# Optimization experiments

Hardware: AMD Instinct MI355X
Metric: run time of the kernel (lower is better)

The kernel has to match this reference:

```python
import jax, jax.numpy as jnp
import numpy as np
from jax import lax

B, T, V = 128, 256, 64
HF = 32   # MLP feature-imputation hidden
CTX = 32  # context hidden
HID = 64  # LSTM hidden


def _uniform(k, shape, fan):
    s = 1.0 / np.sqrt(fan)
    return jax.random.uniform(k, shape, jnp.float32, -s, s)


def setup_inputs():
    key = jax.random.key(0)
    ks = jax.random.split(key, 40)
    values = jax.random.normal(ks[0], (B, T, V), jnp.float32)
    masks = (jax.random.uniform(ks[1], (B, T, V)) > 0.3).astype(jnp.float32)
    deltas = jax.random.uniform(ks[2], (B, T, V), jnp.float32) * 5.0
    lengths = jax.random.randint(ks[3], (B,), T // 2, T + 1)
    min_vals = jnp.min(values, axis=1, keepdims=True)
    max_vals = jnp.max(values, axis=1, keepdims=True)
    D_in = 2 * V + 2 * CTX
    return dict(
        lengths=lengths, values=values, masks=masks, deltas=deltas,
        min_vals=min_vals, max_vals=max_vals,
        W_decay=_uniform(ks[4], (V, V), V), b_decay=_uniform(ks[5], (V,), V),
        W_feat=_uniform(ks[6], (V, HF, V), V), b_feat=_uniform(ks[7], (V, HF), V),
        W_nl1=_uniform(ks[8], (HF, HF), HF), b_nl1=_uniform(ks[9], (HF,), HF),
        W_nl2=_uniform(ks[10], (1, HF), HF), b_nl2=_uniform(ks[11], (1,), HF),
        Wc1=_uniform(ks[12], (2 * CTX, 3 * V + 1), 3 * V + 1), bc1=_uniform(ks[13], (2 * CTX,), 3 * V + 1),
        Wc2=_uniform(ks[14], (CTX, 2 * CTX), 2 * CTX), bc2=_uniform(ks[15], (CTX,), 2 * CTX),
        W_ih_g=_uniform(ks[16], (3 * CTX, 2 * V), CTX), W_hh_g=_uniform(ks[17], (3 * CTX, CTX), CTX),
        b_ih_g=_uniform(ks[18], (3 * CTX,), CTX), b_hh_g=_uniform(ks[19], (3 * CTX,), CTX),
        W_init=_uniform(ks[20], (2 * HID, 2 * CTX), 2 * CTX), b_init=_uniform(ks[21], (2 * HID,), 2 * CTX),
        W_ih_f=_uniform(ks[22], (4 * HID, D_in), HID), W_hh_f=_uniform(ks[23], (4 * HID, HID), HID),
        b_ih_f=_uniform(ks[24], (4 * HID,), HID), b_hh_f=_uniform(ks[25], (4 * HID,), HID),
        W_ih_b=_uniform(ks[26], (4 * HID, D_in), HID), W_hh_b=_uniform(ks[27], (4 * HID, HID), HID),
        b_ih_b=_uniform(ks[28], (4 * HID,), HID), b_hh_b=_uniform(ks[29], (4 * HID,), HID),
        W_ri=_uniform(ks[30], (V, 2 * HID), 2 * HID), b_ri=_uniform(ks[31], (V,), 2 * HID),
        W_fu=_uniform(ks[32], (V, 2 * V), 2 * V), b_fu=_uniform(ks[33], (V,), 2 * V),
    )


def _gru(x, h, Wih, Whh, bih, bhh):
    gi = x @ Wih.T + bih
    gh = h @ Whh.T + bhh
    ir, iz, inn = jnp.split(gi, 3, axis=-1)
    hr, hz, hn = jnp.split(gh, 3, axis=-1)
    r = jax.nn.sigmoid(ir + hr)
    z = jax.nn.sigmoid(iz + hz)
    n = jnp.tanh(inn + r * hn)
    return (1.0 - z) * n + z * h


def _lstm(x, h, c, Wih, Whh, bih, bhh):
    g = x @ Wih.T + bih + h @ Whh.T + bhh
    i, f, gg, o = jnp.split(g, 4, axis=-1)
    c = jax.nn.sigmoid(f) * c + jax.nn.sigmoid(i) * jnp.tanh(gg)
    h = jax.nn.sigmoid(o) * jnp.tanh(c)
    return h, c


def _forward(lengths, values, masks, deltas, min_vals, max_vals,
             W_decay, b_decay, W_feat, b_feat, W_nl1, b_nl1, W_nl2, b_nl2,
             Wc1, bc1, Wc2, bc2, W_ih_g, W_hh_g, b_ih_g, b_hh_g,
             W_init, b_init, W_ih_f, W_hh_f, b_ih_f, b_hh_f,
             W_ih_b, W_hh_b, b_ih_b, b_hh_b, W_ri, b_ri, W_fu, b_fu):
    Bb, Tt, Vv = values.shape
    lf = lengths.astype(jnp.float32)
    pad = (jnp.arange(Tt)[None, :] + 1 <= lengths[:, None]).astype(jnp.float32)  # [B,T]

    msum = masks.sum(axis=1)                       # [B,V] observation counts
    means = values.sum(axis=1) / msum
    var = ((values - means[:, None, :]) ** 2).sum(axis=1) / (msum - 1.0)
    stdev = jnp.sqrt(var)
    missing = 1.0 - msum / lf[:, None]
    stats = jnp.concatenate([lf[:, None], means, stdev, missing], axis=1)  # [B,3V+1]

    mmn = jnp.maximum(max_vals - min_vals, 1e-8)   # [B,1,V]
    nv = (values - min_vals) / mmn
    nmeans = (means - min_vals[:, 0, :]) / mmn[:, 0, :]

    # last-observation-carried-forward x_prime
    nv_tm = jnp.swapaxes(nv, 0, 1)   # [T,B,V]
    m_tm = jnp.swapaxes(masks, 0, 1)

    def pstep(xp, xm):
        x_prev, m_prev = xm
        xp = m_prev * x_prev + (1.0 - m_prev) * xp
        return xp, xp
    _, xp_rest = lax.scan(pstep, nv_tm[0], (nv_tm[:-1], m_tm[:-1]))
    x_prime = jnp.swapaxes(jnp.concatenate([nv_tm[:1], xp_rest], axis=0), 0, 1)

    # InputTemporalDecay: F.linear(d, W*I, b) == d * diag(W) + b
    gamma = jnp.exp(-jax.nn.relu(deltas * jnp.diag(W_decay) + b_decay))
    x_decay = gamma * x_prime + (1.0 - gamma) * nmeans[:, None, :]
    x_complete = masks * nv + (1.0 - masks) * x_decay

    # context vectors
    ctx_mlp = jax.nn.relu(stats @ Wc1.T + bc1) @ Wc2.T + bc2  # [B,CTX]
    x_rnn_tm = jnp.swapaxes(jnp.concatenate([x_complete, masks], axis=-1), 0, 1)  # [T,B,2V]
    pad_tm = jnp.swapaxes(pad, 0, 1)[:, :, None]
    h0 = jnp.zeros((Bb, W_hh_g.shape[1]), values.dtype)

    def gstep(carry, inp):
        h, hn = carry
        x_t, p_t = inp
        h = _gru(x_t, h, W_ih_g, W_hh_g, b_ih_g, b_hh_g)
        hn = p_t * h + (1.0 - p_t) * hn
        return (h, hn), None
    (_, ctx_rnn), _ = lax.scan(gstep, (h0, h0), (x_rnn_tm, pad_tm))
    context = jnp.concatenate([ctx_mlp, ctx_rnn], axis=1)  # [B,2*CTX]

    hinit = context @ W_init.T + b_init  # [B,2H]
    cinit = jnp.tanh(hinit)
    Hh = hinit.shape[1] // 2
    hf0, hb0 = hinit[:, :Hh], hinit[:, Hh:]
    cf0, cb0 = cinit[:, :Hh], cinit[:, Hh:]

    ctx_bt = jnp.broadcast_to(context[:, None, :], (Bb, Tt, context.shape[1]))
    rnn_in_tm = jnp.swapaxes(jnp.concatenate([x_complete, masks, ctx_bt], axis=-1), 0, 1)  # [T,B,D]

    def fstep(carry, x):
        h, c = _lstm(x, carry[0], carry[1], W_ih_f, W_hh_f, b_ih_f, b_hh_f)
        return (h, c), h
    _, hf_rest = lax.scan(fstep, (hf0, cf0), rnn_in_tm[:-1])
    hf_all = jnp.concatenate([hf0[None], hf_rest], axis=0)  # [T,B,H]

    def bstep(carry, x):
        h, c = _lstm(x, carry[0], carry[1], W_ih_b, W_hh_b, b_ih_b, b_hh_b)
        return (h, c), h
    _, hb_rest = lax.scan(bstep, (hb0, cb0), rnn_in_tm[1:][::-1])  # t = T-1 .. 1
    hb_all = jnp.concatenate([hb0[None], hb_rest], axis=0)[::-1]   # time-aligned

    h_cat = jnp.concatenate([hf_all, hb_all], axis=-1)  # [T,B,2H]
    rnn_imp = jnp.swapaxes(h_cat @ W_ri.T + b_ri, 0, 1)  # [B,T,V]

    # per-variable masked feature imputation (no self-connection)
    eye = jnp.eye(Vv, dtype=values.dtype)
    Wm = W_feat * (1.0 - eye[:, None, :])                 # [V,HF,V]
    hidden = jnp.einsum('btv,ghv->btgh', x_complete, Wm) + b_feat  # [B,T,V,HF]
    z = jax.nn.relu(hidden) @ W_nl1.T + b_nl1
    feat_imp = (jax.nn.relu(z) @ W_nl2.T + b_nl2)[..., 0]  # [B,T,V]

    beta = jax.nn.sigmoid(jnp.concatenate([gamma, masks], axis=-1) @ W_fu.T + b_fu)
    final_imp = beta * feat_imp + (1.0 - beta) * rnn_imp

    # unnormalize all three estimates; stack as [3,B,T,V]
    out = jnp.stack([rnn_imp, feat_imp, final_imp], axis=0) * mmn[None] + min_vals[None]
    return out


def reference(lengths, values, masks, deltas, min_vals, max_vals,
              W_decay, b_decay, W_feat, b_feat, W_nl1, b_nl1, W_nl2, b_nl2,
              Wc1, bc1, Wc2, bc2, W_ih_g, W_hh_g, b_ih_g, b_hh_g,
              W_init, b_init, W_ih_f, W_hh_f, b_ih_f, b_hh_f,
              W_ih_b, W_hh_b, b_ih_b, b_hh_b, W_ri, b_ri, W_fu, b_fu):
    return _forward(lengths, values, masks, deltas, min_vals, max_vals,
                    W_decay, b_decay, W_feat, b_feat, W_nl1, b_nl1, W_nl2, b_nl2,
                    Wc1, bc1, Wc2, bc2, W_ih_g, W_hh_g, b_ih_g, b_hh_g,
                    W_init, b_init, W_ih_f, W_hh_f, b_ih_f, b_hh_f,
                    W_ih_b, W_hh_b, b_ih_b, b_hh_b, W_ri, b_ri, W_fu, b_fu)
```

## Files before the change

### kernel.cpp

```cpp
#include <hip/hip_runtime.h>
#include <hip/hip_fp16.h>

static constexpr int NB = 128;
static constexpr int NT = 256;
static constexpr int NV = 64;
static constexpr int NBT = NB * NT;
static constexpr int NBTV = NBT * NV;

typedef __attribute__((ext_vector_type(8))) short short8;
typedef __attribute__((ext_vector_type(4))) float f32x4;
typedef __attribute__((ext_vector_type(4))) float fvec4;

__device__ __forceinline__ void wave_lds_fence() {
    __builtin_amdgcn_sched_barrier(0);
    asm volatile("s_waitcnt lgkmcnt(0)" ::: "memory");
    __builtin_amdgcn_sched_barrier(0);
}

__device__ __forceinline__ void block_sync_lds() {
    __builtin_amdgcn_sched_barrier(0);
    asm volatile("s_waitcnt lgkmcnt(0)" ::: "memory");
    __builtin_amdgcn_s_barrier();
    asm volatile("" ::: "memory");
    __builtin_amdgcn_sched_barrier(0);
}

__device__ __forceinline__ unsigned short f2bf(float x) {
    unsigned int u = __float_as_uint(x);
    return (unsigned short)((u + 0x7FFFu + ((u >> 16) & 1u)) >> 16);
}
__device__ __forceinline__ float bf2f(unsigned short b) {
    return __uint_as_float(((unsigned int)b) << 16);
}
__device__ __forceinline__ unsigned short f2h(float x) {
    union { _Float16 h; unsigned short u; } c; c.h = (_Float16)x; return c.u;
}
__device__ __forceinline__ float fsigm(float x) {
    return __builtin_amdgcn_rcpf(1.0f + __expf(-x));
}
__device__ __forceinline__ float ftanh(float x) {
    return 1.0f - 2.0f * __builtin_amdgcn_rcpf(1.0f + __expf(2.0f * x));
}

__device__ __forceinline__ short8 pack8(float4 a, float4 b) {
    short8 r;
    r[0] = (short)f2bf(a.x); r[1] = (short)f2bf(a.y); r[2] = (short)f2bf(a.z); r[3] = (short)f2bf(a.w);
    r[4] = (short)f2bf(b.x); r[5] = (short)f2bf(b.y); r[6] = (short)f2bf(b.z); r[7] = (short)f2bf(b.w);
    return r;
}

__device__ __forceinline__ void dot4(float4& acc, const float4 wv, const float4 xv) {
    acc.x = fmaf(wv.x, xv.x, acc.x);
    acc.y = fmaf(wv.y, xv.y, acc.y);
    acc.z = fmaf(wv.z, xv.z, acc.z);
    acc.w = fmaf(wv.w, xv.w, acc.w);
}

__global__ __launch_bounds__(256) void k_prep(
    const float* __restrict__ Wf, const float* __restrict__ Wihf,
    const float* __restrict__ Wihb, const float* __restrict__ Wihg,
    const float* __restrict__ Whhf, const float* __restrict__ Whhb,
    const float* __restrict__ Whhg, const float* __restrict__ Wri,
    const float* __restrict__ Wfu,
    unsigned short* __restrict__ wbf, float* __restrict__ wdiag,
    unsigned short* __restrict__ wgf, unsigned short* __restrict__ wgb,
    unsigned short* __restrict__ wgg,
    unsigned short* __restrict__ whhf_h, unsigned short* __restrict__ whhb_h,
    unsigned short* __restrict__ whhg_h,
    unsigned short* __restrict__ wri_bf, unsigned short* __restrict__ wfu_bf) {
    int i = blockIdx.x * 256 + threadIdx.x;
    if (i < NV * 32 * NV) wbf[i] = f2bf(Wf[i]);
    if (i < 2048) wdiag[i] = bf2f(f2bf(Wf[i * 64 + (i >> 5)]));
    if (i < 32768) {
        int n = i >> 7, k = i & 127;
        wgf[i] = f2bf(Wihf[n * 192 + k]);
        wgb[i] = f2bf(Wihb[n * 192 + k]);
    }
    if (i < 12288) wgg[i] = f2bf(Wihg[i]);
    if (i < 16384) { whhf_h[i] = f2h(Whhf[i]); whhb_h[i] = f2h(Whhb[i]); }
    if (i < 3072) whhg_h[i] = f2h(Whhg[i]);
    if (i < 8192) { wri_bf[i] = f2bf(Wri[i]); wfu_bf[i] = f2bf(Wfu[i]); }
}

__global__ __launch_bounds__(256) void k_fill(
    const int* __restrict__ lengths,
    const float* __restrict__ values, const float* __restrict__ masks,
    const float* __restrict__ deltas, const float* __restrict__ minv,
    const float* __restrict__ maxv,
    const float* __restrict__ Wd, const float* __restrict__ bd,
    float* __restrict__ stats,
    float* __restrict__ mmn_ws, float* __restrict__ nmeans_ws,
    float* __restrict__ xcomp, unsigned short* __restrict__ gam,
    const unsigned short* __restrict__ wgg, const float* __restrict__ bihg,
    float* __restrict__ gg) {
    int b = blockIdx.x; int tid = threadIdx.x;
    int v = tid & 63; int tc = tid >> 6;
    float mn = minv[b * NV + v];
    size_t base = (size_t)b * NT * NV + v;
    __shared__ float red[3][4][64];
    __shared__ float lastv[4][64];
    __shared__ int hasf[4][64];
    __shared__ float nv0s[64];
    __shared__ float smm[64], snm[64];
    __shared__ __align__(16) unsigned short sxc[256][64];
    int t0 = tc * 64;
    float sv = 0.f, sq = 0.f, sm = 0.f;
    float last = 0.f; int has = 0;
    for (int t = t0; t < t0 + 64; t++) {
        float val = values[base + (size_t)t * NV];
        float m = masks[base + (size_t)t * NV];
        sv += val; sq += val * val; sm += m;
        if (m != 0.f) { last = val; has = 1; }
        if (tc == 0 && t == 0) nv0s[v] = val;
    }
    red[0][tc][v] = sv; red[1][tc][v] = sq; red[2][tc][v] = sm;
    lastv[tc][v] = last; hasf[tc][v] = has;
    __syncthreads();
    if (tc == 0) {
        sv = red[0][0][v] + red[0][1][v] + red[0][2][v] + red[0][3][v];
        sq = red[1][0][v] + red[1][1][v] + red[1][2][v] + red[1][3][v];
        sm = red[2][0][v] + red[2][1][v] + red[2][2][v] + red[2][3][v];
        float mean = sv / sm;
        float var = (sq - 2.0f * mean * sv + (float)NT * mean * mean) / (sm - 1.0f);
        var = fmaxf(var, 0.0f);
        float sd = sqrtf(var);
        float lf = (float)lengths[b];
        float miss = 1.0f - sm / lf;
        float mx = maxv[b * NV + v];
        float mm = fmaxf(mx - mn, 1e-8f);
        float* st = stats + b * 256;
        if (v == 0) st[0] = lf;
        st[1 + v] = mean; st[65 + v] = sd; st[129 + v] = miss;
        float nmean = (mean - mn) / mm;
        mmn_ws[b * NV + v] = mm;
        nmeans_ws[b * NV + v] = nmean;
        smm[v] = mm; snm[v] = nmean;
    }
    __syncthreads();
    float mm = smm[v];
    float nmean = snm[v];
    float wd = Wd[v * NV + v], bdv = bd[v];
    float xp = (nv0s[v] - mn) / mm;
    for (int q = tc - 1; q >= 0; q--) {
        if (hasf[q][v]) { xp = (lastv[q][v] - mn) / mm; break; }
    }
    for (int t = t0; t < t0 + 64; t++) {
        size_t i = base + (size_t)t * NV;
        float val = values[i], m = masks[i], d = deltas[i];
        float nv = (val - mn) / mm;
        float g = expf(-fmaxf(fmaf(d, wd, bdv), 0.0f));
        float xd = g * xp + (1.0f - g) * nmean;
        float xc = m * nv + (1.0f - m) * xd;
        xcomp[i] = xc; gam[i] = f2bf(g);
        sxc[t][v] = f2bf(xc);
        xp = (m != 0.f) ? nv : xp;
    }
    __syncthreads();
    int lane = tid & 63;
    int r = lane & 15, kc = lane >> 4;
    for (int tile = 0; tile < 4; tile++) {
        int trow = (tc * 4 + tile) * 16;
        int bt0 = b * NT + trow;
        short8 af0 = *(const short8*)&sxc[trow + r][kc * 8];
        short8 af1 = *(const short8*)&sxc[trow + r][32 + kc * 8];
        const float* mr = masks + ((size_t)bt0 + r) * NV + kc * 8;
        short8 af2 = pack8(*(const float4*)(mr), *(const float4*)(mr + 4));
        short8 af3 = pack8(*(const float4*)(mr + 32), *(const float4*)(mr + 36));
        #pragma unroll 3
        for (int nt = 0; nt < 6; nt++) {
            const unsigned short* w = wgg + (size_t)(nt * 16 + r) * 128 + kc * 8;
            float bias = bihg[nt * 16 + r];
            f32x4 acc = {bias, bias, bias, bias};
            acc = __builtin_amdgcn_mfma_f32_16x16x32_bf16(af0, *(const short8*)(w), acc, 0, 0, 0);
            acc = __builtin_amdgcn_mfma_f32_16x16x32_bf16(af1, *(const short8*)(w + 32), acc, 0, 0, 0);
            acc = __builtin_amdgcn_mfma_f32_16x16x32_bf16(af2, *(const short8*)(w + 64), acc, 0, 0, 0);
            acc = __builtin_amdgcn_mfma_f32_16x16x32_bf16(af3, *(const short8*)(w + 96), acc, 0, 0, 0);
            #pragma unroll
            for (int i = 0; i < 4; i++)
                gg[(size_t)(bt0 + kc * 4 + i) * 96 + nt * 16 + r] = acc[i];
        }
    }
}

#define GRU_STEP(T, GIN) { \
    const int t_ = (T); const int p_ = t_ & 1; \
    int4 raw_[4]; \
    const int4* hp_ = (const int4*)hsg[g][s]; \
    _Pragma("unroll") for (int q = 0; q < 4; q++) raw_[q] = hp_[q]; \
    const __half2* hhv_ = (const __half2*)raw_; \
    __half2 a0_ = zh2, a1_ = zh2, a2_ = zh2, a3_ = zh2; \
    _Pragma("unroll") for (int q = 0; q < 16; q += 4) { \
        a0_ = __hfma2(w2[q],     hhv_[q],     a0_); \
        a1_ = __hfma2(w2[q + 1], hhv_[q + 1], a1_); \
        a2_ = __hfma2(w2[q + 2], hhv_[q + 2], a2_); \
        a3_ = __hfma2(w2[q + 3], hhv_[q + 3], a3_); } \
    __half2 sA_ = __hadd2(__hadd2(a0_, a1_), __hadd2(a2_, a3_)); \
    float d_ = __low2float(sA_) + __high2float(sA_); \
    if (g < 2) { \
        gexg[p_][s][n][g] = GIN + bh + d_; \
    } else { \
        gexg[p_][s][n][2] = bh + d_; \
        gexg[p_][s][n][3] = GIN; \
    } \
    block_sync_lds(); \
    float qx_ = gexg[p_][s][n][0], qy_ = gexg[p_][s][n][1]; \
    float qz_ = gexg[p_][s][n][2], qw_ = gexg[p_][s][n][3]; \
    float rr_ = fsigm(qx_); \
    float zz_ = fsigm(qy_); \
    float nn_ = ftanh(qw_ + rr_ * qz_); \
    float h_ = (1.f - zz_) * nn_ + zz_ * hprev; \
    hprev = h_; \
    if (t_ < len) hn = h_; \
    hsg[g][s][n] = f2h(h_); \
    wave_lds_fence(); \
}

#define FEAT_BODY(BT0) { \
    int bt0 = (BT0); \
    int r = lane & 15, kc = lane >> 4; \
    unsigned short* hbw = hbs[wave]; \
    float* lx = ldsx[wave]; \
    float* flw = fls[wave]; \
    short8 a0, a1; \
    { \
        const float* xr = xcomp + (size_t)(bt0 + r) * NV + kc * 8; \
        a0 = pack8(*(const float4*)(xr), *(const float4*)(xr + 4)); \
        a1 = pack8(*(const float4*)(xr + 32), *(const float4*)(xr + 36)); \
    } \
    { \
        int gc0 = kc * 16; \
        const float* xr2 = xcomp + (size_t)(bt0 + r) * NV + gc0; \
        _Pragma("unroll") for (int e = 0; e < 16; e += 4) { \
            float4 p = *(const float4*)(xr2 + e); \
            lx[(gc0 + e + 0) * 16 + r] = bf2f(f2bf(p.x)); \
            lx[(gc0 + e + 1) * 16 + r] = bf2f(f2bf(p.y)); \
            lx[(gc0 + e + 2) * 16 + r] = bf2f(f2bf(p.z)); \
            lx[(gc0 + e + 3) * 16 + r] = bf2f(f2bf(p.w)); \
        } \
    } \
    short8 wb0, wb1; \
    { \
        const float* w = Wnl1 + r * 32 + kc * 8; \
        wb0 = pack8(*(const float4*)w, *(const float4*)(w + 4)); \
        const float* w2p = Wnl1 + (16 + r) * 32 + kc * 8; \
        wb1 = pack8(*(const float4*)w2p, *(const float4*)(w2p + 4)); \
    } \
    float b0i[4], b1i[4], w2a[4], w2b[4]; \
    _Pragma("unroll") for (int i = 0; i < 4; i++) { \
        b0i[i] = bnl1[kc * 4 + i]; \
        b1i[i] = bnl1[16 + kc * 4 + i]; \
        w2a[i] = Wnl2[kc * 4 + i]; \
        w2b[i] = Wnl2[16 + kc * 4 + i]; \
    } \
    float bn2 = bnl2[0]; \
    __builtin_amdgcn_wave_barrier(); \
    _Pragma("unroll 2") for (int g = 0; g < 64; g++) { \
        __builtin_amdgcn_wave_barrier(); \
        float xv[4]; \
        _Pragma("unroll") for (int i = 0; i < 4; i++) xv[i] = lx[g * 16 + kc * 4 + i]; \
        _Pragma("unroll") for (int f = 0; f < 2; f++) { \
            int n0 = g * 32 + f * 16; \
            const unsigned short* wrow = wbf + (size_t)(n0 + r) * 64; \
            short8 b0 = *(const short8*)(wrow + kc * 8); \
            short8 b1 = *(const short8*)(wrow + 32 + kc * 8); \
            f32x4 acc = {0.f, 0.f, 0.f, 0.f}; \
            acc = __builtin_amdgcn_mfma_f32_16x16x32_bf16(a0, b0, acc, 0, 0, 0); \
            acc = __builtin_amdgcn_mfma_f32_16x16x32_bf16(a1, b1, acc, 0, 0, 0); \
            int n = n0 + r; \
            float wd = wdiag[n], bs = bfeat[n]; \
            _Pragma("unroll") for (int i = 0; i < 4; i++) { \
                float h = acc[i] - xv[i] * wd + bs; \
                h = fmaxf(h, 0.0f); \
                hbw[(kc * 4 + i) * 32 + f * 16 + r] = f2bf(h); \
            } \
        } \
        __builtin_amdgcn_wave_barrier(); \
        short8 ah = *(const short8*)(hbw + r * 32 + kc * 8); \
        f32x4 zt0 = {0.f, 0.f, 0.f, 0.f}, zt1 = {0.f, 0.f, 0.f, 0.f}; \
        zt0 = __builtin_amdgcn_mfma_f32_16x16x32_bf16(wb0, ah, zt0, 0, 0, 0); \
        zt1 = __builtin_amdgcn_mfma_f32_16x16x32_bf16(wb1, ah, zt1, 0, 0, 0); \
        float p = 0.f; \
        _Pragma("unroll") for (int i = 0; i < 4; i++) { \
            p = fmaf(fmaxf(zt0[i] + b0i[i], 0.0f), w2a[i], p); \
            p = fmaf(fmaxf(zt1[i] + b1i[i], 0.0f), w2b[i], p); \
        } \
        p += __shfl_xor(p, 16, 64); \
        p += __shfl_xor(p, 32, 64); \
        if (lane < 16) flw[lane * 65 + g] = p + bn2; \
    } \
    __builtin_amdgcn_wave_barrier(); \
    _Pragma("unroll") for (int q = 0; q < 16; q++) \
        feat_out[(size_t)(bt0 + q) * NV + lane] = flw[q * 65 + lane]; \
}

__global__ __launch_bounds__(256, 1) void k_mid(
    const float* __restrict__ gg_t, const int* __restrict__ lengths,
    const unsigned short* __restrict__ whhg_h, const float* __restrict__ bhh,
    float* __restrict__ ctx,
    const float* __restrict__ stats, const float* __restrict__ Wc1,
    const float* __restrict__ bc1, const float* __restrict__ Wc2,
    const float* __restrict__ bc2,
    const float* __restrict__ xcomp, const float* __restrict__ masks,
    const unsigned short* __restrict__ wbf,
    const float* __restrict__ wdiag, const float* __restrict__ bfeat,
    const float* __restrict__ Wnl1, const float* __restrict__ bnl1,
    const float* __restrict__ Wnl2, const float* __restrict__ bnl2,
    float* __restrict__ feat_out,
    const unsigned short* __restrict__ wgf, const unsigned short* __restrict__ wgb,
    float* __restrict__ gf, float* __restrict__ gb) {
    __shared__ __align__(16) unsigned short hsg[3][2][32];
    __shared__ __align__(16) float gexg[2][2][32][5];
    __shared__ __align__(16) float ss[193];
    __shared__ float h1[64];
    __shared__ __align__(16) unsigned short hbs[4][16 * 32];
    __shared__ __align__(16) float ldsx[4][64 * 16];
    __shared__ __align__(16) float fls[4][16 * 65];

    int bx = blockIdx.x;
    int tid = threadIdx.x;

    if (bx < 64) {
        int b0 = bx * 2;
        int g = tid >> 6;
        int lane = tid & 63;
        int s = lane >> 5, n = lane & 31;
        if (g == 3) {
            for (int t = 0; t < NT; t++) block_sync_lds();
            return;
        }
        int b = b0 + s;
        const __half2 zh2 = __float2half2_rn(0.f);
        int4 w4[4];
        {
            const int4* wp = (const int4*)(whhg_h + (size_t)(g * 32 + n) * 32);
            #pragma unroll
            for (int q = 0; q < 4; q++) w4[q] = wp[q];
        }
        const __half2* w2 = (const __half2*)w4;
        float bh = bhh[g * 32 + n];
        int len = lengths[b];
        float hprev = 0.f, hn = 0.f;
        hsg[g][s][n] = f2h(0.f);
        const float* gbase = gg_t + (size_t)b * NT * 96;
        #define GGIDX(T) ((size_t)(T) * 96 + g * 32 + n)
        float gi0 = gbase[GGIDX(0)];
        float gi1 = gbase[GGIDX(1)];
        float gi2 = gbase[GGIDX(2)];
        float gi3 = gbase[GGIDX(3)];
        wave_lds_fence();
        for (int t = 0; t < 252; t += 4) {
            GRU_STEP(t, gi0)
            gi0 = gbase[GGIDX(t + 4)];
            GRU_STEP(t + 1, gi1)
            gi1 = gbase[GGIDX(t + 5)];
            GRU_STEP(t + 2, gi2)
            gi2 = gbase[GGIDX(t + 6)];
            GRU_STEP(t + 3, gi3)
            gi3 = gbase[GGIDX(t + 7)];
        }
        GRU_STEP(252, gi0)
        GRU_STEP(253, gi1)
        GRU_STEP(254, gi2)
        GRU_STEP(255, gi3)
        #undef GGIDX
        if (g == 0) ctx[(b0 + s) * 64 + 32 + n] = hn;
    } else if (bx < 192) {
        if (tid >= 64) return;
        int b = bx - 64;
        ss[tid] = stats[b * 256 + tid];
        ss[64 + tid] = stats[b * 256 + 64 + tid];
        ss[128 + tid] = stats[b * 256 + 128 + tid];
        if (tid == 0) ss[192] = stats[b * 256 + 192];
        wave_lds_fence();
        float acc = bc1[tid];
        const float* w = Wc1 + (size_t)tid * 193;
        for (int k = 0; k < 193; k++) acc = fmaf(w[k], ss[k], acc);
        h1[tid] = fmaxf(acc, 0.f);
        wave_lds_fence();
        if (tid < 32) {
            float a = bc2[tid];
            const float* w2 = Wc2 + tid * 64;
            for (int k = 0; k < 64; k++) a = fmaf(w2[k], h1[k], a);
            ctx[b * 64 + tid] = a;
        }
    } else if (bx < 448) {
        int wave = tid >> 6; int lane = tid & 63;
        FEAT_BODY((bx - 192) * 64 + wave * 16)
    } else {
        int wave = tid >> 6, lane = tid & 63;
        int bt0 = (bx - 448) * 64 + wave * 16;
        int r = lane & 15, kc = lane >> 4;
        const float* xr = xcomp + (size_t)(bt0 + r) * NV + kc * 8;
        const float* mr = masks + (size_t)(bt0 + r) * NV + kc * 8;
        short8 af0 = pack8(*(const float4*)(xr), *(const float4*)(xr + 4));
        short8 af1 = pack8(*(const float4*)(xr + 32), *(const float4*)(xr + 36));
        short8 af2 = pack8(*(const float4*)(mr), *(const float4*)(mr + 4));
        short8 af3 = pack8(*(const float4*)(mr + 32), *(const float4*)(mr + 36));
        #pragma unroll 4
        for (int nt = 0; nt < 16; nt++) {
            const unsigned short* w = wgf + (size_t)(nt * 16 + r) * 128 + kc * 8;
            f32x4 acc = {0.f, 0.f, 0.f, 0.f};
            acc = __builtin_amdgcn_mfma_f32_16x16x32_bf16(af0, *(const short8*)(w), acc, 0, 0, 0);
            acc = __builtin_amdgcn_mfma_f32_16x16x32_bf16(af1, *(const short8*)(w + 32), acc, 0, 0, 0);
            acc = __builtin_amdgcn_mfma_f32_16x16x32_bf16(af2, *(const short8*)(w + 64), acc, 0, 0, 0);
            acc = __builtin_amdgcn_mfma_f32_16x16x32_bf16(af3, *(const short8*)(w + 96), acc, 0, 0, 0);
            int col = nt * 16 + r;
            #pragma unroll
            for (int i = 0; i < 4; i++)
                gf[(size_t)(bt0 + kc * 4 + i) * 256 + col] = acc[i];
        }
        #pragma unroll 4
        for (int nt = 0; nt < 16; nt++) {
            const unsigned short* w = wgb + (size_t)(nt * 16 + r) * 128 + kc * 8;
            f32x4 acc = {0.f, 0.f, 0.f, 0.f};
            acc = __builtin_amdgcn_mfma_f32_16x16x32_bf16(af0, *(const short8*)(w), acc, 0, 0, 0);
            acc = __builtin_amdgcn_mfma_f32_16x16x32_bf16(af1, *(const short8*)(w + 32), acc, 0, 0, 0);
            acc = __builtin_amdgcn_mfma_f32_16x16x32_bf16(af2, *(const short8*)(w + 64), acc, 0, 0, 0);
            acc = __builtin_amdgcn_mfma_f32_16x16x32_bf16(af3, *(const short8*)(w + 96), acc, 0, 0, 0);
            int col = nt * 16 + r;
            #pragma unroll
            for (int i = 0; i < 4; i++)
                gb[(size_t)(bt0 + kc * 4 + i) * 256 + col] = acc[i];
        }
    }
}

#define LSTM_STEP(S, GIN) { \
    const int s_ = (S); const int p_ = s_ & 1; \
    int4 raw_[8]; \
    const int4* hp_ = (const int4*)hs[g]; \
    _Pragma("unroll") for (int q = 0; q < 8; q++) raw_[q] = hp_[q]; \
    const __half2* hhv_ = (const __half2*)raw_; \
    __half2 a0_ = zh2, a1_ = zh2, a2_ = zh2, a3_ = zh2; \
    _Pragma("unroll") for (int q = 0; q < 32; q += 4) { \
        a0_ = __hfma2(w2[q],     hhv_[q],     a0_); \
        a1_ = __hfma2(w2[q + 1], hhv_[q + 1], a1_); \
        a2_ = __hfma2(w2[q + 2], hhv_[q + 2], a2_); \
        a3_ = __hfma2(w2[q + 3], hhv_[q + 3], a3_); } \
    __half2 sA_ = __hadd2(__hadd2(a0_, a1_), __hadd2(a2_, a3_)); \
    float d_ = __low2float(sA_) + __high2float(sA_); \
    gex[p_][n][g] = GIN + ctg + d_; \
    block_sync_lds(); \
    float qx_ = gex[p_][n][0], qy_ = gex[p_][n][1]; \
    float qz_ = gex[p_][n][2], qw_ = gex[p_][n][3]; \
    float ii_ = fsigm(qx_); \
    float ff_ = fsigm(qy_); \
    float gv_ = ftanh(qz_); \
    float oo_ = fsigm(qw_); \
    c = ff_ * c + ii_ * gv_; \
    float hv_ = oo_ * ftanh(c); \
    if (g == 0) { \
        int tout_ = dir ? (NT - 2 - s_) : (s_ + 1); \
        hall[((size_t)b * NT + tout_) * NV + n] = hv_; \
    } \
    hs[g][n] = f2h(hv_); \
    wave_lds_fence(); \
}

__global__ __launch_bounds__(256, 1) void k_lstm(
    const float* __restrict__ gf, const float* __restrict__ gb,
    const float* __restrict__ ctx,
    const unsigned short* __restrict__ whhf_h, const unsigned short* __restrict__ whhb_h,
    const float* __restrict__ Wihf, const float* __restrict__ Wihb,
    const float* __restrict__ bihf, const float* __restrict__ bhhf,
    const float* __restrict__ bihb, const float* __restrict__ bhhb,
    const float* __restrict__ Wini, const float* __restrict__ bini,
    float* __restrict__ out0, float* __restrict__ out1,
    const float* __restrict__ xcomp, const unsigned short* __restrict__ wbf,
    const float* __restrict__ wdiag, const float* __restrict__ bfeat,
    const float* __restrict__ Wnl1, const float* __restrict__ bnl1,
    const float* __restrict__ Wnl2, const float* __restrict__ bnl2,
    float* __restrict__ feat_out) {
    __shared__ __align__(16) unsigned short hs[4][64];
    __shared__ __align__(16) float gex[2][64][5];
    __shared__ __align__(16) float sctx[64];
    __shared__ __align__(16) float sh0[64];
    __shared__ __align__(16) unsigned short hbs[4][16 * 32];
    __shared__ __align__(16) float ldsx[4][64 * 16];
    __shared__ __align__(16) float fls[4][16 * 65];

    int bx = blockIdx.x;
    int tid = threadIdx.x;

    if (bx >= 256) {
        int wave = tid >> 6; int lane = tid & 63;
        FEAT_BODY((bx - 256) * 64 + 16384 + wave * 16)
        return;
    }

    int dir = bx >> 7; int b = bx & 127;
    int g = tid >> 6;
    int n = tid & 63;
    const float* gates = dir ? gb : gf;
    const unsigned short* wsrc = dir ? whhb_h : whhf_h;
    float* hall = dir ? out1 : out0;
    const __half2 zh2 = __float2half2_rn(0.f);
    int4 w4[8];
    {
        const int4* wp = (const int4*)(wsrc + (size_t)(g * 64 + n) * 64);
        #pragma unroll
        for (int q = 0; q < 8; q++) w4[q] = wp[q];
    }
    const __half2* w2 = (const __half2*)w4;
    size_t gbase = (size_t)b * NT * 256 + tid;
    #define GIDX(S) (gbase + (size_t)(dir ? (NT - 1 - (S)) : (S)) * 256)
    float gi0 = gates[GIDX(0)];
    float gi1 = gates[GIDX(1)];
    float gi2 = gates[GIDX(2)];
    float gi3 = gates[GIDX(3)];
    if (tid < 64) sctx[tid] = ctx[b * 64 + tid];
    __syncthreads();
    float ctg;
    {
        const float4* wc = (const float4*)((dir ? Wihb : Wihf) + (size_t)tid * 192 + 128);
        float bias = dir ? (bihb[tid] + bhhb[tid]) : (bihf[tid] + bhhf[tid]);
        const float4* c4 = (const float4*)sctx;
        float4 a = {0, 0, 0, 0};
        #pragma unroll
        for (int q = 0; q < 16; q++) dot4(a, wc[q], c4[q]);
        ctg = bias + a.x + a.y + a.z + a.w;
    }
    if (tid < 64) {
        const float4* wi = (const float4*)(Wini + (size_t)(dir * 64 + tid) * 64);
        const float4* c4 = (const float4*)sctx;
        float4 a = {0, 0, 0, 0};
        #pragma unroll
        for (int q = 0; q < 16; q++) dot4(a, wi[q], c4[q]);
        sh0[tid] = bini[dir * 64 + tid] + a.x + a.y + a.z + a.w;
    }
    __syncthreads();
    float c;
    {
        float h0 = sh0[n];
        c = ftanh(h0);
        hs[g][n] = f2h(h0);
        if (g == 0) {
            int t0 = dir ? (NT - 1) : 0;
            hall[((size_t)b * NT + t0) * NV + n] = h0;
        }
    }
    wave_lds_fence();
    for (int sx = 0; sx < 252; sx += 4) {
        LSTM_STEP(sx, gi0)
        gi0 = gates[GIDX(sx + 4)];
        LSTM_STEP(sx + 1, gi1)
        gi1 = gates[GIDX(sx + 5)];
        LSTM_STEP(sx + 2, gi2)
        gi2 = gates[GIDX(sx + 6)];
        LSTM_STEP(sx + 3, gi3)
        gi3 = gates[GIDX(sx + 7)];
    }
    LSTM_STEP(252, gi0)
    LSTM_STEP(253, gi1)
    LSTM_STEP(254, gi2)
    #undef GIDX
}

__global__ __launch_bounds__(256) void k_post(
    const unsigned short* __restrict__ gam, const float* __restrict__ masks,
    const unsigned short* __restrict__ wri_bf, const unsigned short* __restrict__ wfu_bf,
    const float* __restrict__ bri, const float* __restrict__ bfu,
    const float* __restrict__ mmn_ws, const float* __restrict__ minv,
    float* out0, float* out1, float* out2) {
    int wave = threadIdx.x >> 6, lane = threadIdx.x & 63;
    int bt0 = blockIdx.x * 64 + wave * 16;
    int r = lane & 15, kc = lane >> 4;
    int b = bt0 >> 8;
    const float* h0r = out0 + (size_t)(bt0 + r) * NV + kc * 8;
    const float* h1r = out1 + (size_t)(bt0 + r) * NV + kc * 8;
    const unsigned short* gr = gam + (size_t)(bt0 + r) * NV + kc * 8;
    const float* mr  = masks + (size_t)(bt0 + r) * NV + kc * 8;
    short8 A0 = pack8(*(const float4*)(h0r), *(const float4*)(h0r + 4));
    short8 A1 = pack8(*(const float4*)(h0r + 32), *(const float4*)(h0r + 36));
    short8 A2 = pack8(*(const float4*)(h1r), *(const float4*)(h1r + 4));
    short8 A3 = pack8(*(const float4*)(h1r + 32), *(const float4*)(h1r + 36));
    short8 G0 = *(const short8*)(gr);
    short8 G1 = *(const short8*)(gr + 32);
    short8 M0 = pack8(*(const float4*)(mr), *(const float4*)(mr + 4));
    short8 M1 = pack8(*(const float4*)(mr + 32), *(const float4*)(mr + 36));
    #pragma unroll
    for (int nt = 0; nt < 4; nt++) {
        int n = nt * 16 + r;
        const unsigned short* wr = wri_bf + (size_t)n * 128 + kc * 8;
        const unsigned short* wf = wfu_bf + (size_t)n * 128 + kc * 8;
        float bi = bri[n], bf_ = bfu[n];
        f32x4 racc = {bi, bi, bi, bi};
        f32x4 bacc = {bf_, bf_, bf_, bf_};
        racc = __builtin_amdgcn_mfma_f32_16x16x32_bf16(A0, *(const short8*)(wr), racc, 0, 0, 0);
        racc = __builtin_amdgcn_mfma_f32_16x16x32_bf16(A1, *(const short8*)(wr + 32), racc, 0, 0, 0);
        racc = __builtin_amdgcn_mfma_f32_16x16x32_bf16(A2, *(const short8*)(wr + 64), racc, 0, 0, 0);
        racc = __builtin_amdgcn_mfma_f32_16x16x32_bf16(A3, *(const short8*)(wr + 96), racc, 0, 0, 0);
        bacc = __builtin_amdgcn_mfma_f32_16x16x32_bf16(G0, *(const short8*)(wf), bacc, 0, 0, 0);
        bacc = __builtin_amdgcn_mfma_f32_16x16x32_bf16(G1, *(const short8*)(wf + 32), bacc, 0, 0, 0);
        bacc = __builtin_amdgcn_mfma_f32_16x16x32_bf16(M0, *(const short8*)(wf + 64), bacc, 0, 0, 0);
        bacc = __builtin_amdgcn_mfma_f32_16x16x32_bf16(M1, *(const short8*)(wf + 96), bacc, 0, 0, 0);
        float mm = mmn_ws[b * NV + n], mn = minv[b * NV + n];
        #pragma unroll
        for (int i = 0; i < 4; i++) {
            int row = bt0 + kc * 4 + i;
            size_t idx = (size_t)row * NV + n;
            float rn = racc[i];
            float beta = fsigm(bacc[i]);
            float ft = out2[idx];
            float fin = beta * ft + (1.0f - beta) * rn;
            out0[idx] = fmaf(rn, mm, mn);
            out1[idx] = fmaf(ft, mm, mn);
            out2[idx] = fmaf(fin, mm, mn);
        }
    }
}

extern "C" void kernel_launch(void* const* d_in, const int* in_sizes, int n_in,
                              void* d_out, int out_size, void* d_ws, size_t ws_size,
                              hipStream_t stream) {
    const int*   lengths  = (const int*)d_in[0];
    const float* values   = (const float*)d_in[1];
    const float* masks    = (const float*)d_in[2];
    const float* deltas   = (const float*)d_in[3];
    const float* min_vals = (const float*)d_in[4];
    const float* max_vals = (const float*)d_in[5];
    const float* W_decay  = (const float*)d_in[6];
    const float* b_decay  = (const float*)d_in[7];
    const float* W_feat   = (const float*)d_in[8];
    const float* b_feat   = (const float*)d_in[9];
    const float* W_nl1    = (const float*)d_in[10];
    const float* b_nl1    = (const float*)d_in[11];
    const float* W_nl2    = (const float*)d_in[12];
    const float* b_nl2    = (const float*)d_in[13];
    const float* Wc1      = (const float*)d_in[14];
    const float* bc1      = (const float*)d_in[15];
    const float* Wc2      = (const float*)d_in[16];
    const float* bc2      = (const float*)d_in[17];
    const float* W_ih_g   = (const float*)d_in[18];
    const float* W_hh_g   = (const float*)d_in[19];
    const float* b_ih_g   = (const float*)d_in[20];
    const float* b_hh_g   = (const float*)d_in[21];
    const float* W_init   = (const float*)d_in[22];
    const float* b_init   = (const float*)d_in[23];
    const float* W_ih_f   = (const float*)d_in[24];
    const float* W_hh_f   = (const float*)d_in[25];
    const float* b_ih_f   = (const float*)d_in[26];
    const float* b_hh_f   = (const float*)d_in[27];
    const float* W_ih_b   = (const float*)d_in[28];
    const float* W_hh_b   = (const float*)d_in[29];
    const float* b_ih_b   = (const float*)d_in[30];
    const float* b_hh_b   = (const float*)d_in[31];
    const float* W_ri     = (const float*)d_in[32];
    const float* b_ri     = (const float*)d_in[33];
    const float* W_fu     = (const float*)d_in[34];
    const float* b_fu     = (const float*)d_in[35];

    float* ws = (float*)d_ws;
    float* xcomp  = ws;
    unsigned short* gam = (unsigned short*)(ws + 2097152);
    unsigned short* wri_bf = (unsigned short*)(ws + 4194304);
    unsigned short* wfu_bf = (unsigned short*)(ws + 4198400);
    float* stats  = ws + 6291456;
    float* mmn    = ws + 6324224;
    float* nmeans = ws + 6332416;
    float* ctx    = ws + 6340608;
    unsigned short* wbf = (unsigned short*)(ws + 6365184);
    float* wdiag  = ws + 6430720;
    unsigned short* wgf = (unsigned short*)(ws + 6432768);
    unsigned short* wgb = (unsigned short*)(ws + 6449152);
    unsigned short* wgg = (unsigned short*)(ws + 6465536);
    unsigned short* whhf_h = (unsigned short*)(ws + 6471680);
    unsigned short* whhb_h = (unsigned short*)(ws + 6479872);
    unsigned short* whhg_h = (unsigned short*)(ws + 6488064);
    float* gates_f = ws + 6555136;
    float* gates_b = ws + 14943744;
    float* gates_g = ws + 23332352;

    float* out0 = (float*)d_out;
    float* out1 = out0 + NBTV;
    float* out2 = out0 + 2 * NBTV;

    k_prep<<<512, 256, 0, stream>>>(W_feat, W_ih_f, W_ih_b, W_ih_g, W_hh_f, W_hh_b, W_hh_g,
                                    W_ri, W_fu,
                                    wbf, wdiag, wgf, wgb, wgg, whhf_h, whhb_h, whhg_h,
                                    wri_bf, wfu_bf);
    k_fill<<<NB, 256, 0, stream>>>(lengths, values, masks, deltas, min_vals, max_vals,
                                   W_decay, b_decay, stats, mmn, nmeans, xcomp, gam,
                                   wgg, b_ih_g, gates_g);
    k_mid<<<960, 256, 0, stream>>>(gates_g, lengths, whhg_h, b_hh_g, ctx,
                                   stats, Wc1, bc1, Wc2, bc2,
                                   xcomp, masks, wbf, wdiag, b_feat, W_nl1, b_nl1, W_nl2, b_nl2, out2,
                                   wgf, wgb, gates_f, gates_b);
    k_lstm<<<512, 256, 0, stream>>>(gates_f, gates_b, ctx, whhf_h, whhb_h,
                                    W_ih_f, W_ih_b, b_ih_f, b_hh_f, b_ih_b, b_hh_b,
                                    W_init, b_init, out0, out1,
                                    xcomp, wbf, wdiag, b_feat, W_nl1, b_nl1, W_nl2, b_nl2, out2);
    k_post<<<NBT / 64, 256, 0, stream>>>(gam, masks, wri_bf, wfu_bf, b_ri, b_fu, mmn, min_vals,
                                         out0, out1, out2);
}
```

Baseline: 251.4 us.

## Fuse forward and backward LSTM directions into one block per batch

```diff
diff --git a/kernel.cpp b/kernel.cpp
--- a/kernel.cpp
+++ b/kernel.cpp
@@ -425,35 +425,50 @@
     }
 }
 
-#define LSTM_STEP(S, GIN) { \
+#define LSTM_STEP_D(S, GI0, GI1) { \
     const int s_ = (S); const int p_ = s_ & 1; \
-    int4 raw_[8]; \
-    const int4* hp_ = (const int4*)hs[g]; \
-    _Pragma("unroll") for (int q = 0; q < 8; q++) raw_[q] = hp_[q]; \
-    const __half2* hhv_ = (const __half2*)raw_; \
+    int4 raw0_[8], raw1_[8]; \
+    const int4* hp0_ = (const int4*)hs[g][0]; \
+    const int4* hp1_ = (const int4*)hs[g][1]; \
+    _Pragma("unroll") for (int q = 0; q < 8; q++) { raw0_[q] = hp0_[q]; raw1_[q] = hp1_[q]; } \
+    const __half2* h0v_ = (const __half2*)raw0_; \
+    const __half2* h1v_ = (const __half2*)raw1_; \
     __half2 a0_ = zh2, a1_ = zh2, a2_ = zh2, a3_ = zh2; \
+    __half2 b0_ = zh2, b1_ = zh2, b2_ = zh2, b3_ = zh2; \
     _Pragma("unroll") for (int q = 0; q < 32; q += 4) { \
-        a0_ = __hfma2(w2[q],     hhv_[q],     a0_); \
-        a1_ = __hfma2(w2[q + 1], hhv_[q + 1], a1_); \
-        a2_ = __hfma2(w2[q + 2], hhv_[q + 2], a2_); \
-        a3_ = __hfma2(w2[q + 3], hhv_[q + 3], a3_); } \
+        a0_ = __hfma2(w2f[q],     h0v_[q],     a0_); \
+        a1_ = __hfma2(w2f[q + 1], h0v_[q + 1], a1_); \
+        a2_ = __hfma2(w2f[q + 2], h0v_[q + 2], a2_); \
+        a3_ = __hfma2(w2f[q + 3], h0v_[q + 3], a3_); \
+        b0_ = __hfma2(w2b[q],     h1v_[q],     b0_); \
+        b1_ = __hfma2(w2b[q + 1], h1v_[q + 1], b1_); \
+        b2_ = __hfma2(w2b[q + 2], h1v_[q + 2], b2_); \
+        b3_ = __hfma2(w2b[q + 3], h1v_[q + 3], b3_); } \
     __half2 sA_ = __hadd2(__hadd2(a0_, a1_), __hadd2(a2_, a3_)); \
-    float d_ = __low2float(sA_) + __high2float(sA_); \
-    gex[p_][n][g] = GIN + ctg + d_; \
+    __half2 sB_ = __hadd2(__hadd2(b0_, b1_), __hadd2(b2_, b3_)); \
+    float d0_ = __low2float(sA_) + __high2float(sA_); \
+    float d1_ = __low2float(sB_) + __high2float(sB_); \
+    gex[p_][0][n][g] = GI0 + ctg0 + d0_; \
+    gex[p_][1][n][g] = GI1 + ctg1 + d1_; \
     block_sync_lds(); \
-    float qx_ = gex[p_][n][0], qy_ = gex[p_][n][1]; \
-    float qz_ = gex[p_][n][2], qw_ = gex[p_][n][3]; \
-    float ii_ = fsigm(qx_); \
-    float ff_ = fsigm(qy_); \
-    float gv_ = ftanh(qz_); \
-    float oo_ = fsigm(qw_); \
-    c = ff_ * c + ii_ * gv_; \
-    float hv_ = oo_ * ftanh(c); \
+    float qx0_ = gex[p_][0][n][0], qy0_ = gex[p_][0][n][1]; \
+    float qz0_ = gex[p_][0][n][2], qw0_ = gex[p_][0][n][3]; \
+    float qx1_ = gex[p_][1][n][0], qy1_ = gex[p_][1][n][1]; \
+    float qz1_ = gex[p_][1][n][2], qw1_ = gex[p_][1][n][3]; \
+    float ii0_ = fsigm(qx0_), ii1_ = fsigm(qx1_); \
+    float ff0_ = fsigm(qy0_), ff1_ = fsigm(qy1_); \
+    float gv0_ = ftanh(qz0_), gv1_ = ftanh(qz1_); \
+    float oo0_ = fsigm(qw0_), oo1_ = fsigm(qw1_); \
+    c0 = ff0_ * c0 + ii0_ * gv0_; \
+    c1 = ff1_ * c1 + ii1_ * gv1_; \
+    float hv0_ = oo0_ * ftanh(c0); \
+    float hv1_ = oo1_ * ftanh(c1); \
     if (g == 0) { \
-        int tout_ = dir ? (NT - 2 - s_) : (s_ + 1); \
-        hall[((size_t)b * NT + tout_) * NV + n] = hv_; \
+        out0[((size_t)b * NT + (s_ + 1)) * NV + n] = hv0_; \
+        out1[((size_t)b * NT + (NT - 2 - s_)) * NV + n] = hv1_; \
     } \
-    hs[g][n] = f2h(hv_); \
+    hs[g][0][n] = f2h(hv0_); \
+    hs[g][1][n] = f2h(hv1_); \
     wave_lds_fence(); \
 }
 
@@ -471,10 +486,10 @@
     const float* __restrict__ Wnl1, const float* __restrict__ bnl1,
     const float* __restrict__ Wnl2, const float* __restrict__ bnl2,
     float* __restrict__ feat_out) {
-    __shared__ __align__(16) unsigned short hs[4][64];
-    __shared__ __align__(16) float gex[2][64][5];
+    __shared__ __align__(16) unsigned short hs[4][2][64];
+    __shared__ __align__(16) float gex[2][2][64][5];
     __shared__ __align__(16) float sctx[64];
-    __shared__ __align__(16) float sh0[64];
+    __shared__ __align__(16) float sh0[128];
     __shared__ __align__(16) unsigned short hbs[4][16 * 32];
     __shared__ __align__(16) float ldsx[4][64 * 16];
     __shared__ __align__(16) float fls[4][16 * 65];
@@ -482,78 +497,87 @@
     int bx = blockIdx.x;
     int tid = threadIdx.x;
 
-    if (bx >= 256) {
+    if (bx >= 128) {
         int wave = tid >> 6; int lane = tid & 63;
-        FEAT_BODY((bx - 256) * 64 + 16384 + wave * 16)
+        FEAT_BODY((bx - 128) * 64 + 16384 + wave * 16)
         return;
     }
 
-    int dir = bx >> 7; int b = bx & 127;
+    int b = bx;
     int g = tid >> 6;
     int n = tid & 63;
-    const float* gates = dir ? gb : gf;
-    const unsigned short* wsrc = dir ? whhb_h : whhf_h;
-    float* hall = dir ? out1 : out0;
     const __half2 zh2 = __float2half2_rn(0.f);
-    int4 w4[8];
+    int4 w4f[8], w4b[8];
     {
-        const int4* wp = (const int4*)(wsrc + (size_t)(g * 64 + n) * 64);
+        const int4* wpf = (const int4*)(whhf_h + (size_t)(g * 64 + n) * 64);
+        const int4* wpb = (const int4*)(whhb_h + (size_t)(g * 64 + n) * 64);
         #pragma unroll
-        for (int q = 0; q < 8; q++) w4[q] = wp[q];
-    }
-    const __half2* w2 = (const __half2*)w4;
-    size_t gbase = (size_t)b * NT * 256 + tid;
-    #define GIDX(S) (gbase + (size_t)(dir ? (NT - 1 - (S)) : (S)) * 256)
-    float gi0 = gates[GIDX(0)];
-    float gi1 = gates[GIDX(1)];
-    float gi2 = gates[GIDX(2)];
-    float gi3 = gates[GIDX(3)];
+        for (int q = 0; q < 8; q++) { w4f[q] = wpf[q]; w4b[q] = wpb[q]; }
+    }
+    const __half2* w2f = (const __half2*)w4f;
+    const __half2* w2b = (const __half2*)w4b;
+    size_t gbf = (size_t)b * NT * 256 + tid;
+    #define GIDX0(S) (gbf + (size_t)(S) * 256)
+    #define GIDX1(S) (gbf + (size_t)(NT - 1 - (S)) * 256)
+    float gi0_0 = gf[GIDX0(0)], gi0_1 = gb[GIDX1(0)];
+    float gi1_0 = gf[GIDX0(1)], gi1_1 = gb[GIDX1(1)];
+    float gi2_0 = gf[GIDX0(2)], gi2_1 = gb[GIDX1(2)];
+    float gi3_0 = gf[GIDX0(3)], gi3_1 = gb[GIDX1(3)];
     if (tid < 64) sctx[tid] = ctx[b * 64 + tid];
     __syncthreads();
-    float ctg;
+    float ctg0, ctg1;
     {
-        const float4* wc = (const float4*)((dir ? Wihb : Wihf) + (size_t)tid * 192 + 128);
-        float bias = dir ? (bihb[tid] + bhhb[tid]) : (bihf[tid] + bhhf[tid]);
         const float4* c4 = (const float4*)sctx;
-        float4 a = {0, 0, 0, 0};
+        const float4* wcf = (const float4*)(Wihf + (size_t)tid * 192 + 128);
+        const float4* wcb = (const float4*)(Wihb + (size_t)tid * 192 + 128);
+        float4 af = {0, 0, 0, 0}, ab = {0, 0, 0, 0};
         #pragma unroll
-        for (int q = 0; q < 16; q++) dot4(a, wc[q], c4[q]);
-        ctg = bias + a.x + a.y + a.z + a.w;
-    }
-    if (tid < 64) {
-        const float4* wi = (const float4*)(Wini + (size_t)(dir * 64 + tid) * 64);
+        for (int q = 0; q < 16; q++) {
+            float4 cv = c4[q];
+            dot4(af, wcf[q], cv);
+            dot4(ab, wcb[q], cv);
+        }
+        ctg0 = bihf[tid] + bhhf[tid] + af.x + af.y + af.z + af.w;
+        ctg1 = bihb[tid] + bhhb[tid] + ab.x + ab.y + ab.z + ab.w;
+    }
+    if (tid < 128) {
+        const float4* wi = (const float4*)(Wini + (size_t)tid * 64);
         const float4* c4 = (const float4*)sctx;
         float4 a = {0, 0, 0, 0};
         #pragma unroll
         for (int q = 0; q < 16; q++) dot4(a, wi[q], c4[q]);
-        sh0[tid] = bini[dir * 64 + tid] + a.x + a.y + a.z + a.w;
+        sh0[tid] = bini[tid] + a.x + a.y + a.z + a.w;
     }
     __syncthreads();
-    float c;
+    float c0, c1;
     {
-        float h0 = sh0[n];
-        c = ftanh(h0);
-        hs[g][n] = f2h(h0);
+        float h00 = sh0[n];
+        float h01 = sh0[64 + n];
+        c0 = ftanh(h00);
+        c1 = ftanh(h01);
+        hs[g][0][n] = f2h(h00);
+        hs[g][1][n] = f2h(h01);
         if (g == 0) {
-            int t0 = dir ? (NT - 1) : 0;
-            hall[((size_t)b * NT + t0) * NV + n] = h0;
+            out0[((size_t)b * NT + 0) * NV + n] = h00;
+            out1[((size_t)b * NT + (NT - 1)) * NV + n] = h01;
         }
     }
     wave_lds_fence();
     for (int sx = 0; sx < 252; sx += 4) {
-        LSTM_STEP(sx, gi0)
-        gi0 = gates[GIDX(sx + 4)];
-        LSTM_STEP(sx + 1, gi1)
-        gi1 = gates[GIDX(sx + 5)];
-        LSTM_STEP(sx + 2, gi2)
-        gi2 = gates[GIDX(sx + 6)];
-        LSTM_STEP(sx + 3, gi3)
-        gi3 = gates[GIDX(sx + 7)];
-    }
-    LSTM_STEP(252, gi0)
-    LSTM_STEP(253, gi1)
-    LSTM_STEP(254, gi2)
-    #undef GIDX
+        LSTM_STEP_D(sx, gi0_0, gi0_1)
+        gi0_0 = gf[GIDX0(sx + 4)]; gi0_1 = gb[GIDX1(sx + 4)];
+        LSTM_STEP_D(sx + 1, gi1_0, gi1_1)
+        gi1_0 = gf[GIDX0(sx + 5)]; gi1_1 = gb[GIDX1(sx + 5)];
+        LSTM_STEP_D(sx + 2, gi2_0, gi2_1)
+        gi2_0 = gf[GIDX0(sx + 6)]; gi2_1 = gb[GIDX1(sx + 6)];
+        LSTM_STEP_D(sx + 3, gi3_0, gi3_1)
+        gi3_0 = gf[GIDX0(sx + 7)]; gi3_1 = gb[GIDX1(sx + 7)];
+    }
+    LSTM_STEP_D(252, gi0_0, gi0_1)
+    LSTM_STEP_D(253, gi1_0, gi1_1)
+    LSTM_STEP_D(254, gi2_0, gi2_1)
+    #undef GIDX0
+    #undef GIDX1
 }
 
 __global__ __launch_bounds__(256) void k_post(
@@ -686,7 +710,7 @@
                                    stats, Wc1, bc1, Wc2, bc2,
                                    xcomp, masks, wbf, wdiag, b_feat, W_nl1, b_nl1, W_nl2, b_nl2, out2,
                                    wgf, wgb, gates_f, gates_b);
-    k_lstm<<<512, 256, 0, stream>>>(gates_f, gates_b, ctx, whhf_h, whhb_h,
+    k_lstm<<<384, 256, 0, stream>>>(gates_f, gates_b, ctx, whhf_h, whhb_h,
                                     W_ih_f, W_ih_b, b_ih_f, b_hh_f, b_ih_b, b_hh_b,
                                     W_init, b_init, out0, out1,
                                     xcomp, wbf, wdiag, b_feat, W_nl1, b_nl1, W_nl2, b_nl2, out2);
```

After: 311.9 us. +24.0%, slower.
